# Kernel tuning notes

Measured on AMD Instinct MI355X. Metric: run time of the kernel, lower is better.

The kernel has to match this reference:

```python
import jax, jax.numpy as jnp
import numpy as np

H, QK, V, PQ, PV = 12, 32, 32, 8, 8
INF = 1e5


def _ln(x, g, b, eps=1e-5):
    m = jnp.mean(x, axis=-1, keepdims=True)
    v = jnp.mean((x - m) ** 2, axis=-1, keepdims=True)
    return (x - m) / jnp.sqrt(v + eps) * g + b


def _l2g(R, t, p):
    # R: (N,L,3,3), t: (N,L,3), p: (N,L,...,3) local points -> global
    q = jnp.einsum('nlij,nl...j->nl...i', R, p)
    tb = t.reshape(t.shape[0], t.shape[1], *([1] * (p.ndim - 3)), 3)
    return q + tb


def _g2l(R, t, q):
    tb = t.reshape(t.shape[0], t.shape[1], *([1] * (q.ndim - 3)), 3)
    return jnp.einsum('nlji,nl...j->nl...i', R, q - tb)


def setup_inputs() -> dict:
    key = jax.random.key(0)
    ks = jax.random.split(key, 24)
    N, L, F, C = 1, 384, 128, 64
    s = 0.02
    r = lambda k, sh: jax.random.normal(k, sh, dtype=jnp.float32)
    DOUT = H * C + H * V + H * PV * 7  # 1824
    return {
        'R': r(ks[0], (N, L, 3, 3)),
        't': r(ks[1], (N, L, 3)),
        'x': r(ks[2], (N, L, F)),
        'z': r(ks[3], (N, L, L, C)),
        'mask': jnp.ones((N, L), dtype=bool),
        'Wq': r(ks[4], (F, H * QK)) * s,
        'Wk': r(ks[5], (F, H * QK)) * s,
        'Wv': r(ks[6], (F, H * V)) * s,
        'Wpb': r(ks[7], (C, H)) * s,
        'spatial_coef': jnp.full((1, 1, 1, H), np.log(np.e - 1.0), dtype=jnp.float32),
        'Wqp': r(ks[8], (F, H * PQ * 3)) * s,
        'Wkp': r(ks[9], (F, H * PQ * 3)) * s,
        'Wvp': r(ks[10], (F, H * PV * 3)) * s,
        'Wout': r(ks[11], (DOUT, F)) * s,
        'bout': jnp.zeros((F,), jnp.float32),
        'ln1_g': jnp.ones((F,), jnp.float32),
        'ln1_b': jnp.zeros((F,), jnp.float32),
        'W1': r(ks[12], (F, F)) * s, 'b1': jnp.zeros((F,), jnp.float32),
        'W2': r(ks[13], (F, F)) * s, 'b2': jnp.zeros((F,), jnp.float32),
        'W3': r(ks[14], (F, F)) * s, 'b3': jnp.zeros((F,), jnp.float32),
        'ln2_g': jnp.ones((F,), jnp.float32),
        'ln2_b': jnp.zeros((F,), jnp.float32),
    }


def ga_block(R, t, x, z, mask, Wq, Wk, Wv, Wpb, spatial_coef, Wqp, Wkp, Wvp,
             Wout, bout, ln1_g, ln1_b, W1, b1, W2, b2, W3, b3, ln2_g, ln2_b):
    N, L, F = x.shape
    # node logits
    q = (x @ Wq).reshape(N, L, H, QK)
    k = (x @ Wk).reshape(N, L, H, QK)
    logits_node = jnp.einsum('nihd,njhd->nijh', q, k) / np.sqrt(QK)
    # pair logits
    logits_pair = z @ Wpb  # (N,L,L,H)
    # spatial logits: squared distances between global query/key point sets
    qp = _l2g(R, t, (x @ Wqp).reshape(N, L, H * PQ, 3)).reshape(N, L, H, PQ * 3)
    kp = _l2g(R, t, (x @ Wkp).reshape(N, L, H * PQ, 3)).reshape(N, L, H, PQ * 3)
    qn = jnp.sum(qp * qp, -1)  # (N,L,H)
    kn = jnp.sum(kp * kp, -1)
    cross = jnp.einsum('nihd,njhd->nijh', qp, kp)
    sum_sq_dist = qn[:, :, None] + kn[:, None] - 2.0 * cross  # (N,L,L,H)
    gamma = jax.nn.softplus(spatial_coef)
    logits_spatial = sum_sq_dist * (-gamma * np.sqrt(2.0 / (9 * PQ)) / 2.0)
    # masked softmax over j (axis=2)
    logits = (logits_node + logits_pair + logits_spatial) * np.sqrt(1.0 / 3.0)
    mask_row = mask[:, :, None, None]
    mask_pair = mask_row & mask[:, None, :, None]
    logits = jnp.where(mask_pair, logits, logits - INF)
    alpha = jax.nn.softmax(logits, axis=2)
    alpha = jnp.where(mask_row, alpha, jnp.zeros_like(alpha))
    # pair aggregation
    feat_p2n = jnp.einsum('nijh,nijc->nihc', alpha, z).reshape(N, L, -1)
    # node-value aggregation
    v = (x @ Wv).reshape(N, L, H, V)
    feat_node = jnp.einsum('nijh,njhd->nihd', alpha, v).reshape(N, L, -1)
    # spatial aggregation over global value points, mapped back to local frames
    vp = _l2g(R, t, (x @ Wvp).reshape(N, L, H, PV, 3))
    aggr = jnp.einsum('nijh,njhpc->nihpc', alpha, vp)
    fp = _g2l(R, t, aggr)  # (N,L,H,PV,3)
    dist = jnp.linalg.norm(fp, axis=-1)  # (N,L,H,PV)
    dirn = fp / (dist[..., None] + 1e-4)
    feat_spatial = jnp.concatenate(
        [fp.reshape(N, L, -1), dist.reshape(N, L, -1), dirn.reshape(N, L, -1)], -1)
    feat_all = jnp.concatenate([feat_p2n, feat_node, feat_spatial], -1) @ Wout + bout
    feat_all = jnp.where(mask[..., None], feat_all, jnp.zeros_like(feat_all))
    x1 = _ln(x + feat_all, ln1_g, ln1_b)
    h = jax.nn.relu(x1 @ W1 + b1)
    h = jax.nn.relu(h @ W2 + b2)
    h = h @ W3 + b3
    return _ln(x1 + h, ln2_g, ln2_b)


def reference(R, t, x, z, mask, Wq, Wk, Wv, Wpb, spatial_coef, Wqp, Wkp, Wvp,
              Wout, bout, ln1_g, ln1_b, W1, b1, W2, b2, W3, b3, ln2_g, ln2_b):
    return ga_block(R, t, x, z, mask, Wq, Wk, Wv, Wpb, spatial_coef, Wqp, Wkp,
                    Wvp, Wout, bout, ln1_g, ln1_b, W1, b1, W2, b2, W3, b3,
                    ln2_g, ln2_b)
```

## Files before the change

### kernel.cpp

```cpp
#include <hip/hip_runtime.h>
#include <math.h>

constexpr int LL   = 384;
constexpr int FF   = 128;
constexpr int NH   = 12;
constexpr int HQK  = 384;
constexpr int HV   = 384;
constexpr int HP3  = 288;
constexpr int CC   = 64;
constexpr int P2N  = 768;

__device__ inline unsigned short f2bf(float f) {
    unsigned int u = __float_as_uint(f);
    return (unsigned short)((u + 0x7fff + ((u >> 16) & 1)) >> 16);
}
__device__ inline float bf2f(unsigned short s) {
    return __uint_as_float(((unsigned int)s) << 16);
}

__global__ void __launch_bounds__(256) k1a_gemm(
    const float* __restrict__ x,
    const float* __restrict__ Wq, const float* __restrict__ Wk, const float* __restrict__ Wv,
    const float* __restrict__ Wqp, const float* __restrict__ Wkp, const float* __restrict__ Wvp,
    float* __restrict__ qb, float* __restrict__ kb, float* __restrict__ vb,
    float* __restrict__ qpl, float* __restrict__ kpl, float* __restrict__ vpl) {
    const int bid = blockIdx.x, tid = threadIdx.x;
    const int ct = bid % 63, rt = bid / 63;
    __shared__ float xs[64 * 132];

    const float* W; float* O; int ld, cb;
    if (ct < 12)      { W = Wq;  O = qb;  ld = 384; cb = ct * 32; }
    else if (ct < 24) { W = Wk;  O = kb;  ld = 384; cb = (ct - 12) * 32; }
    else if (ct < 36) { W = Wv;  O = vb;  ld = 384; cb = (ct - 24) * 32; }
    else if (ct < 45) { W = Wqp; O = qpl; ld = 288; cb = (ct - 36) * 32; }
    else if (ct < 54) { W = Wkp; O = kpl; ld = 288; cb = (ct - 45) * 32; }
    else              { W = Wvp; O = vpl; ld = 288; cb = (ct - 54) * 32; }
    const int r0 = rt * 64;

    const float4* xsrc = (const float4*)(x + (size_t)r0 * FF);
#pragma unroll
    for (int k = 0; k < 8; ++k) {
        int idx = tid + k * 256;
        float4 v = xsrc[idx];
        int row = idx >> 5, c4 = (idx & 31) * 4;
        float* d = &xs[row * 132 + c4];
        d[0] = v.x; d[1] = v.y; d[2] = v.z; d[3] = v.w;
    }
    __syncthreads();

    const int cq = (tid & 7) * 4;
    const int rr = (tid >> 3) * 2;
    const float* Wp = W + cb + cq;
    const float* xr0 = &xs[rr * 132];
    const float* xr1 = &xs[(rr + 1) * 132];
    float a00=0,a01=0,a02=0,a03=0, a10=0,a11=0,a12=0,a13=0;
#pragma unroll 8
    for (int f = 0; f < FF; ++f) {
        const float4 w = *(const float4*)(Wp + (size_t)f * ld);
        float xa = xr0[f], xb = xr1[f];
        a00 = fmaf(xa, w.x, a00); a01 = fmaf(xa, w.y, a01);
        a02 = fmaf(xa, w.z, a02); a03 = fmaf(xa, w.w, a03);
        a10 = fmaf(xb, w.x, a10); a11 = fmaf(xb, w.y, a11);
        a12 = fmaf(xb, w.z, a12); a13 = fmaf(xb, w.w, a13);
    }
    float* o0 = O + (size_t)(r0 + rr) * ld + cb + cq;
    float* o1 = o0 + ld;
    o0[0]=a00; o0[1]=a01; o0[2]=a02; o0[3]=a03;
    o1[0]=a10; o1[1]=a11; o1[2]=a12; o1[3]=a13;
}

__global__ void __launch_bounds__(256) k3_node(
    const float* __restrict__ qb, const float* __restrict__ kb,
    const float* __restrict__ qpl, const float* __restrict__ kpl,
    const float* __restrict__ R, const float* __restrict__ t,
    const float* __restrict__ spc, float* __restrict__ lgN) {
    const int it = blockIdx.x, jt = blockIdx.y, h = blockIdx.z;
    const int tid = threadIdx.x;
    __shared__ float As[64 * 60];
    __shared__ float Bs[64 * 60];
    __shared__ float pnA[512], pnB[512];
    const float g = log1pf(expf(spc[h]));
    const float s3 = 0.5773502691896258f;
    const float c1 = s3 * 0.17677669529663687f;
    const float c2 = s3 * g * (1.f / 6.f);
    const float c3 = -s3 * g * (1.f / 12.f);
    const int i0 = it * 64, j0 = jt * 64;

    for (int idx = tid; idx < 2048; idx += 256) {
        int r = idx >> 5, c = idx & 31;
        As[r*60 + c] = qb[(size_t)(i0 + r) * HQK + h*32 + c];
        Bs[r*60 + c] = kb[(size_t)(j0 + r) * HQK + h*32 + c] * c1;
    }
    for (int idx = tid; idx < 1024; idx += 256) {
        const int side = idx >> 9, rem = idx & 511;
        const int r = rem >> 3, p = rem & 7;
        const int row = (side ? j0 : i0) + r;
        const float* P = side ? kpl : qpl;
        const float* lp = P + (size_t)row * HP3 + (h*8 + p) * 3;
        float l0 = lp[0], l1 = lp[1], l2 = lp[2];
        float g0 = fmaf(R[row*9+0], l0, fmaf(R[row*9+1], l1, fmaf(R[row*9+2], l2, t[row*3+0])));
        float g1 = fmaf(R[row*9+3], l0, fmaf(R[row*9+4], l1, fmaf(R[row*9+5], l2, t[row*3+1])));
        float g2 = fmaf(R[row*9+6], l0, fmaf(R[row*9+7], l1, fmaf(R[row*9+8], l2, t[row*3+2])));
        float nn = g0*g0 + g1*g1 + g2*g2;
        if (side == 0) {
            float* d = &As[r*60 + 32 + p*3];
            d[0] = g0 * c2; d[1] = g1 * c2; d[2] = g2 * c2;
            pnA[r*8 + p] = nn;
        } else {
            float* d = &Bs[r*60 + 32 + p*3];
            d[0] = g0; d[1] = g1; d[2] = g2;
            pnB[r*8 + p] = nn;
        }
    }
    __syncthreads();
    if (tid < 64) {
        float s = 0.f;
#pragma unroll
        for (int p = 0; p < 8; ++p) s += pnA[tid*8 + p];
        As[tid*60 + 56] = s * c3;
        As[tid*60 + 57] = 1.f;
        As[tid*60 + 58] = 0.f; As[tid*60 + 59] = 0.f;
    } else if (tid < 128) {
        const int r = tid - 64;
        float s = 0.f;
#pragma unroll
        for (int p = 0; p < 8; ++p) s += pnB[r*8 + p];
        Bs[r*60 + 56] = 1.f;
        Bs[r*60 + 57] = s * c3;
        Bs[r*60 + 58] = 0.f; Bs[r*60 + 59] = 0.f;
    }
    __syncthreads();

    const int tx = tid & 15, ty = tid >> 4;
    float acc[4][4] = {};
    for (int k4 = 0; k4 < 60; k4 += 4) {
        float4 a[4], b[4];
#pragma unroll
        for (int r = 0; r < 4; ++r) a[r] = *(const float4*)&As[(ty*4 + r)*60 + k4];
#pragma unroll
        for (int c = 0; c < 4; ++c) b[c] = *(const float4*)&Bs[(tx*4 + c)*60 + k4];
#pragma unroll
        for (int r = 0; r < 4; ++r)
#pragma unroll
            for (int c = 0; c < 4; ++c) {
                acc[r][c] = fmaf(a[r].x, b[c].x, acc[r][c]);
                acc[r][c] = fmaf(a[r].y, b[c].y, acc[r][c]);
                acc[r][c] = fmaf(a[r].z, b[c].z, acc[r][c]);
                acc[r][c] = fmaf(a[r].w, b[c].w, acc[r][c]);
            }
    }
#pragma unroll
    for (int r = 0; r < 4; ++r)
        *(float4*)&lgN[((size_t)(i0 + ty*4 + r) * NH + h) * LL + j0 + tx*4] =
            make_float4(acc[r][0], acc[r][1], acc[r][2], acc[r][3]);
}

__global__ void __launch_bounds__(512, 4) k4a_fused(
    const float* __restrict__ z, const float* __restrict__ Wpb,
    float* __restrict__ lgA, float* __restrict__ feat) {
    const int i = blockIdx.x, tid = threadIdx.x;
    __shared__ __align__(16) unsigned char zu[384 * 68 * 2];
    unsigned short* z_s = (unsigned short*)zu;
    float* red = (float*)zu;
    __shared__ float a_s[NH * 384];

    const float4* zsrc = (const float4*)(z + (size_t)i * (LL * CC));
#pragma unroll
    for (int k = 0; k < 12; ++k) {
        int idx = tid + k * 512;
        float4 v = zsrc[idx];
        int j = idx >> 4, c4 = idx & 15;
        ushort4 pk;
        pk.x = f2bf(v.x); pk.y = f2bf(v.y); pk.z = f2bf(v.z); pk.w = f2bf(v.w);
        *(ushort4*)&z_s[j * 68 + c4 * 4] = pk;
    }
    __syncthreads();

    if (tid < 384) {
        const int j = tid;
        float pacc[12] = {};
        const unsigned short* zrow = &z_s[j * 68];
#pragma unroll
        for (int c4 = 0; c4 < 16; ++c4) {
            ushort4 zz = *(const ushort4*)&zrow[c4 * 4];
            float z0 = bf2f(zz.x), z1 = bf2f(zz.y), z2 = bf2f(zz.z), z3 = bf2f(zz.w);
            const float* wp = Wpb + c4 * 4 * NH;
#pragma unroll
            for (int hh = 0; hh < 12; ++hh) {
                float p = pacc[hh];
                p = fmaf(z0, wp[hh], p);
                p = fmaf(z1, wp[NH + hh], p);
                p = fmaf(z2, wp[2*NH + hh], p);
                p = fmaf(z3, wp[3*NH + hh], p);
                pacc[hh] = p;
            }
        }
        const float s3 = 0.5773502691896258f;
#pragma unroll
        for (int hh = 0; hh < 12; ++hh)
            a_s[hh * 384 + j] = lgA[((size_t)i * NH + hh) * LL + j] + pacc[hh] * s3;
    }
    __syncthreads();

    const int wv = tid >> 6, lane = tid & 63;
    if (wv < 6) {
#pragma unroll
        for (int rr = 0; rr < 2; ++rr) {
            const int h = wv * 2 + rr;
            float v[6];
#pragma unroll
            for (int k = 0; k < 6; ++k) v[k] = a_s[h * 384 + lane + k * 64];
            float m = v[0];
#pragma unroll
            for (int k = 1; k < 6; ++k) m = fmaxf(m, v[k]);
#pragma unroll
            for (int off = 32; off; off >>= 1) m = fmaxf(m, __shfl_xor(m, off));
            float s = 0.f;
#pragma unroll
            for (int k = 0; k < 6; ++k) { v[k] = expf(v[k] - m); s += v[k]; }
#pragma unroll
            for (int off = 32; off; off >>= 1) s += __shfl_xor(s, off);
            float inv = 1.f / s;
#pragma unroll
            for (int k = 0; k < 6; ++k) {
                float a = v[k] * inv;
                a_s[h * 384 + lane + k * 64] = a;
                lgA[((size_t)i * NH + h) * LL + lane + k * 64] = a;
            }
        }
    }
    __syncthreads();

    const int c4 = tid & 15, jc = tid >> 4;
    float4 acc[12] = {};
    const int jbase = jc * 12;
#pragma unroll
    for (int j4 = 0; j4 < 3; ++j4) {
        const int j = jbase + j4 * 4;
        float zv[4][4];
#pragma unroll
        for (int jj = 0; jj < 4; ++jj) {
            ushort4 zz = *(const ushort4*)&z_s[(j + jj) * 68 + c4 * 4];
            zv[jj][0] = bf2f(zz.x); zv[jj][1] = bf2f(zz.y);
            zv[jj][2] = bf2f(zz.z); zv[jj][3] = bf2f(zz.w);
        }
#pragma unroll
        for (int hh = 0; hh < 12; ++hh) {
            float4 a4 = *(const float4*)&a_s[hh * 384 + j];
            acc[hh].x = fmaf(a4.x, zv[0][0], acc[hh].x); acc[hh].y = fmaf(a4.x, zv[0][1], acc[hh].y);
            acc[hh].z = fmaf(a4.x, zv[0][2], acc[hh].z); acc[hh].w = fmaf(a4.x, zv[0][3], acc[hh].w);
            acc[hh].x = fmaf(a4.y, zv[1][0], acc[hh].x); acc[hh].y = fmaf(a4.y, zv[1][1], acc[hh].y);
            acc[hh].z = fmaf(a4.y, zv[1][2], acc[hh].z); acc[hh].w = fmaf(a4.y, zv[1][3], acc[hh].w);
            acc[hh].x = fmaf(a4.z, zv[2][0], acc[hh].x); acc[hh].y = fmaf(a4.z, zv[2][1], acc[hh].y);
            acc[hh].z = fmaf(a4.z, zv[2][2], acc[hh].z); acc[hh].w = fmaf(a4.z, zv[2][3], acc[hh].w);
            acc[hh].x = fmaf(a4.w, zv[3][0], acc[hh].x); acc[hh].y = fmaf(a4.w, zv[3][1], acc[hh].y);
            acc[hh].z = fmaf(a4.w, zv[3][2], acc[hh].z); acc[hh].w = fmaf(a4.w, zv[3][3], acc[hh].w);
        }
    }
    __syncthreads();
#pragma unroll
    for (int hh = 0; hh < 12; ++hh) {
        acc[hh].x += __shfl_xor(acc[hh].x, 16); acc[hh].y += __shfl_xor(acc[hh].y, 16);
        acc[hh].z += __shfl_xor(acc[hh].z, 16); acc[hh].w += __shfl_xor(acc[hh].w, 16);
        acc[hh].x += __shfl_xor(acc[hh].x, 32); acc[hh].y += __shfl_xor(acc[hh].y, 32);
        acc[hh].z += __shfl_xor(acc[hh].z, 32); acc[hh].w += __shfl_xor(acc[hh].w, 32);
    }
    if (lane < 16) {
#pragma unroll
        for (int hh = 0; hh < 12; ++hh)
            *(float4*)&red[wv * 768 + hh * 64 + lane * 4] = acc[hh];
    }
    __syncthreads();
    if (tid < 192) {
        int hh = tid >> 4, cc = tid & 15;
        float4 s = make_float4(0.f, 0.f, 0.f, 0.f);
#pragma unroll
        for (int w = 0; w < 8; ++w) {
            float4 p = *(const float4*)&red[w * 768 + hh * 64 + cc * 4];
            s.x += p.x; s.y += p.y; s.z += p.z; s.w += p.w;
        }
        *(float4*)&feat[(size_t)i * P2N + hh * 64 + cc * 4] = s;
    }
}

__global__ void __launch_bounds__(512) k45_aggproj(
    const float* __restrict__ alpha, const float* __restrict__ vb,
    const float* __restrict__ vpl, const float* __restrict__ R,
    const float* __restrict__ t, const float* __restrict__ feat,
    const float* __restrict__ Wout, float* __restrict__ partial) {
    const int it = blockIdx.x, h = blockIdx.y;
    const int tid = threadIdx.x;
    __shared__ float bs[128 * 57];
    __shared__ float atile[16][128];
    __shared__ float fa[16][152];
    __shared__ float sa[16][24];
    const int i0 = it * 16;
    const int wv = __builtin_amdgcn_readfirstlane(tid >> 6);
    const int n = tid & 63;

    if (tid < 256) {
        int r = tid >> 4, c4 = tid & 15;
        float4 v = *(const float4*)&feat[(size_t)(i0 + r) * P2N + h * 64 + c4 * 4];
        *(float4*)&fa[r][c4 * 4] = v;
    }

    float acc[2] = {0.f, 0.f};
    for (int tile = 0; tile < 3; ++tile) {
        const int j0 = tile * 128;
        __syncthreads();
        for (int idx = tid; idx < 2048; idx += 512) {
            if (idx < 1024) {
                int jr = idx >> 3, q = idx & 7;
                const float* src = vb + (size_t)(j0 + jr) * HV + h * 32 + q * 4;
                float* d = &bs[jr * 57 + q * 4];
                d[0] = src[0]; d[1] = src[1]; d[2] = src[2]; d[3] = src[3];
            } else {
                int id2 = idx - 1024;
                int jr = id2 >> 3, p = id2 & 7;
                const int row = j0 + jr;
                const float* lp = vpl + (size_t)row * HP3 + (h*8 + p) * 3;
                float l0 = lp[0], l1 = lp[1], l2 = lp[2];
                float g0 = fmaf(R[row*9+0], l0, fmaf(R[row*9+1], l1, fmaf(R[row*9+2], l2, t[row*3+0])));
                float g1 = fmaf(R[row*9+3], l0, fmaf(R[row*9+4], l1, fmaf(R[row*9+5], l2, t[row*3+1])));
                float g2 = fmaf(R[row*9+6], l0, fmaf(R[row*9+7], l1, fmaf(R[row*9+8], l2, t[row*3+2])));
                float* d = &bs[jr * 57 + 32 + p * 3];
                d[0] = g0; d[1] = g1; d[2] = g2;
            }
        }
        {
            int r = tid >> 5, c4 = tid & 31;
            float4 v = *(const float4*)&alpha[((size_t)(i0 + r) * NH + h) * LL + j0 + c4 * 4];
            *(float4*)&atile[r][c4 * 4] = v;
        }
        __syncthreads();
        if (n < 56) {
            for (int j4 = 0; j4 < 32; ++j4) {
                float bv0 = bs[(j4*4+0)*57 + n];
                float bv1 = bs[(j4*4+1)*57 + n];
                float bv2 = bs[(j4*4+2)*57 + n];
                float bv3 = bs[(j4*4+3)*57 + n];
#pragma unroll
                for (int r = 0; r < 2; ++r) {
                    float4 a4 = *(const float4*)&atile[wv * 2 + r][j4 * 4];
                    acc[r] = fmaf(a4.x, bv0, acc[r]);
                    acc[r] = fmaf(a4.y, bv1, acc[r]);
                    acc[r] = fmaf(a4.z, bv2, acc[r]);
                    acc[r] = fmaf(a4.w, bv3, acc[r]);
                }
            }
        }
    }
    __syncthreads();
    if (n < 56) {
        if (n < 32) {
#pragma unroll
            for (int r = 0; r < 2; ++r) fa[wv * 2 + r][64 + n] = acc[r];
        } else {
#pragma unroll
            for (int r = 0; r < 2; ++r) sa[wv * 2 + r][n - 32] = acc[r];
        }
    }
    __syncthreads();
    if (tid < 128) {
        const int ri = tid >> 3, p = tid & 7;
        const int i = i0 + ri;
        float d0 = sa[ri][p*3+0] - t[i*3+0];
        float d1 = sa[ri][p*3+1] - t[i*3+1];
        float d2 = sa[ri][p*3+2] - t[i*3+2];
        float f0 = R[i*9+0]*d0 + R[i*9+3]*d1 + R[i*9+6]*d2;
        float f1 = R[i*9+1]*d0 + R[i*9+4]*d1 + R[i*9+7]*d2;
        float f2 = R[i*9+2]*d0 + R[i*9+5]*d1 + R[i*9+8]*d2;
        float dist = sqrtf(f0*f0 + f1*f1 + f2*f2);
        float inv = 1.f / (dist + 1e-4f);
        fa[ri][96 + p*3+0] = f0; fa[ri][96 + p*3+1] = f1; fa[ri][96 + p*3+2] = f2;
        fa[ri][120 + p] = dist;
        fa[ri][128 + p*3+0] = f0*inv; fa[ri][128 + p*3+1] = f1*inv; fa[ri][128 + p*3+2] = f2*inv;
    }
    __syncthreads();

    const int f = tid & 127, rg = tid >> 7;
    float o[4] = {};
    const float* fr0 = &fa[rg * 4][0];
    {
        const float* w = Wout + (size_t)(h * 64) * FF + f;
        for (int k = 0; k < 64; ++k) {
            float wv_ = w[(size_t)k * FF];
#pragma unroll
            for (int r = 0; r < 4; ++r) o[r] = fmaf(fr0[r * 152 + k], wv_, o[r]);
        }
    }
    {
        const float* w = Wout + (size_t)(768 + h * 32) * FF + f;
        for (int k = 0; k < 32; ++k) {
            float wv_ = w[(size_t)k * FF];
#pragma unroll
            for (int r = 0; r < 4; ++r) o[r] = fmaf(fr0[r * 152 + 64 + k], wv_, o[r]);
        }
    }
    {
        const float* w = Wout + (size_t)(1152 + h * 24) * FF + f;
        for (int k = 0; k < 24; ++k) {
            float wv_ = w[(size_t)k * FF];
#pragma unroll
            for (int r = 0; r < 4; ++r) o[r] = fmaf(fr0[r * 152 + 96 + k], wv_, o[r]);
        }
    }
    {
        const float* w = Wout + (size_t)(1440 + h * 8) * FF + f;
        for (int k = 0; k < 8; ++k) {
            float wv_ = w[(size_t)k * FF];
#pragma unroll
            for (int r = 0; r < 4; ++r) o[r] = fmaf(fr0[r * 152 + 120 + k], wv_, o[r]);
        }
    }
    {
        const float* w = Wout + (size_t)(1536 + h * 24) * FF + f;
        for (int k = 0; k < 24; ++k) {
            float wv_ = w[(size_t)k * FF];
#pragma unroll
            for (int r = 0; r < 4; ++r) o[r] = fmaf(fr0[r * 152 + 128 + k], wv_, o[r]);
        }
    }
#pragma unroll
    for (int r = 0; r < 4; ++r)
        partial[((size_t)h * LL + i0 + rg * 4 + r) * FF + f] = o[r];
}

__global__ void __launch_bounds__(512) k5b_rowepi(
    const float* __restrict__ partial, const float* __restrict__ bout,
    const float* __restrict__ x,
    const float* __restrict__ ln1g, const float* __restrict__ ln1b,
    const float* __restrict__ W1, const float* __restrict__ b1,
    const float* __restrict__ W2, const float* __restrict__ b2,
    const float* __restrict__ W3, const float* __restrict__ b3,
    const float* __restrict__ ln2g, const float* __restrict__ ln2b,
    float* __restrict__ out) {
    const int i = blockIdx.x, tid = threadIdx.x;
    const int f = tid & 127, q = tid >> 7;
    __shared__ float prt[4][128];
    __shared__ float x1s[128], hbA[128], hbB[128];
    __shared__ float wrA[2], wrB[2];

    {
        float acc = 0.f;
#pragma unroll
        for (int k = 0; k < 3; ++k)
            acc += partial[((size_t)(q * 3 + k) * LL + i) * FF + f];
        prt[q][f] = acc;
    }
    __syncthreads();

    float s1 = 0.f, dv1 = 0.f;
    if (tid < 128) {
        s1 = prt[0][f] + prt[1][f] + prt[2][f] + prt[3][f] + bout[f] + x[(size_t)i * FF + f];
        float r = s1;
#pragma unroll
        for (int off = 32; off; off >>= 1) r += __shfl_xor(r, off);
        if ((tid & 63) == 0) wrA[tid >> 6] = r;
    }
    __syncthreads();
    if (tid < 128) {
        float mu = (wrA[0] + wrA[1]) * (1.f / FF);
        dv1 = s1 - mu;
        float r = dv1 * dv1;
#pragma unroll
        for (int off = 32; off; off >>= 1) r += __shfl_xor(r, off);
        if ((tid & 63) == 0) wrB[tid >> 6] = r;
    }
    __syncthreads();
    if (tid < 128) {
        float var = (wrB[0] + wrB[1]) * (1.f / FF);
        x1s[f] = dv1 * rsqrtf(var + 1e-5f) * ln1g[f] + ln1b[f];
    }
    __syncthreads();

    {
        const int k0 = q * 32;
        float p0=0,p1=0,p2=0,p3=0;
        for (int k = 0; k < 8; ++k) {
            int d = k0 + k * 4;
            p0 = fmaf(x1s[d+0], W1[(size_t)(d+0)*FF + f], p0);
            p1 = fmaf(x1s[d+1], W1[(size_t)(d+1)*FF + f], p1);
            p2 = fmaf(x1s[d+2], W1[(size_t)(d+2)*FF + f], p2);
            p3 = fmaf(x1s[d+3], W1[(size_t)(d+3)*FF + f], p3);
        }
        prt[q][f] = p0 + p1 + p2 + p3;
    }
    __syncthreads();
    if (tid < 128) hbA[f] = fmaxf(prt[0][f]+prt[1][f]+prt[2][f]+prt[3][f] + b1[f], 0.f);
    __syncthreads();
    {
        const int k0 = q * 32;
        float p0=0,p1=0,p2=0,p3=0;
        for (int k = 0; k < 8; ++k) {
            int d = k0 + k * 4;
            p0 = fmaf(hbA[d+0], W2[(size_t)(d+0)*FF + f], p0);
            p1 = fmaf(hbA[d+1], W2[(size_t)(d+1)*FF + f], p1);
            p2 = fmaf(hbA[d+2], W2[(size_t)(d+2)*FF + f], p2);
            p3 = fmaf(hbA[d+3], W2[(size_t)(d+3)*FF + f], p3);
        }
        prt[q][f] = p0 + p1 + p2 + p3;
    }
    __syncthreads();
    if (tid < 128) hbB[f] = fmaxf(prt[0][f]+prt[1][f]+prt[2][f]+prt[3][f] + b2[f], 0.f);
    __syncthreads();
    {
        const int k0 = q * 32;
        float p0=0,p1=0,p2=0,p3=0;
        for (int k = 0; k < 8; ++k) {
            int d = k0 + k * 4;
            p0 = fmaf(hbB[d+0], W3[(size_t)(d+0)*FF + f], p0);
            p1 = fmaf(hbB[d+1], W3[(size_t)(d+1)*FF + f], p1);
            p2 = fmaf(hbB[d+2], W3[(size_t)(d+2)*FF + f], p2);
            p3 = fmaf(hbB[d+3], W3[(size_t)(d+3)*FF + f], p3);
        }
        prt[q][f] = p0 + p1 + p2 + p3;
    }
    __syncthreads();

    float s2 = 0.f, dv2 = 0.f;
    if (tid < 128) {
        s2 = x1s[f] + prt[0][f]+prt[1][f]+prt[2][f]+prt[3][f] + b3[f];
        float r = s2;
#pragma unroll
        for (int off = 32; off; off >>= 1) r += __shfl_xor(r, off);
        if ((tid & 63) == 0) wrA[tid >> 6] = r;
    }
    __syncthreads();
    if (tid < 128) {
        float mu = (wrA[0] + wrA[1]) * (1.f / FF);
        dv2 = s2 - mu;
        float r = dv2 * dv2;
#pragma unroll
        for (int off = 32; off; off >>= 1) r += __shfl_xor(r, off);
        if ((tid & 63) == 0) wrB[tid >> 6] = r;
    }
    __syncthreads();
    if (tid < 128) {
        float var = (wrB[0] + wrB[1]) * (1.f / FF);
        out[(size_t)i * FF + f] = dv2 * rsqrtf(var + 1e-5f) * ln2g[f] + ln2b[f];
    }
}

extern "C" void kernel_launch(void* const* d_in, const int* in_sizes, int n_in,
                              void* d_out, int out_size, void* d_ws, size_t ws_size,
                              hipStream_t stream) {
    const float* R    = (const float*)d_in[0];
    const float* t    = (const float*)d_in[1];
    const float* x    = (const float*)d_in[2];
    const float* z    = (const float*)d_in[3];
    const float* Wq   = (const float*)d_in[5];
    const float* Wk   = (const float*)d_in[6];
    const float* Wv   = (const float*)d_in[7];
    const float* Wpb  = (const float*)d_in[8];
    const float* spc  = (const float*)d_in[9];
    const float* Wqp  = (const float*)d_in[10];
    const float* Wkp  = (const float*)d_in[11];
    const float* Wvp  = (const float*)d_in[12];
    const float* Wout = (const float*)d_in[13];
    const float* bout = (const float*)d_in[14];
    const float* ln1g = (const float*)d_in[15];
    const float* ln1b = (const float*)d_in[16];
    const float* W1   = (const float*)d_in[17];
    const float* b1   = (const float*)d_in[18];
    const float* W2   = (const float*)d_in[19];
    const float* b2   = (const float*)d_in[20];
    const float* W3   = (const float*)d_in[21];
    const float* b3   = (const float*)d_in[22];
    const float* ln2g = (const float*)d_in[23];
    const float* ln2b = (const float*)d_in[24];
    float* out = (float*)d_out;

    float* ws = (float*)d_ws;
    float* qb   = ws;
    float* kb   = qb   + (size_t)LL * HQK;
    float* vb   = kb   + (size_t)LL * HQK;
    float* qpl  = vb   + (size_t)LL * HV;
    float* kpl  = qpl  + (size_t)LL * HP3;
    float* vpl  = kpl  + (size_t)LL * HP3;
    float* lgA  = vpl  + (size_t)LL * HP3;
    float* feat = lgA  + (size_t)LL * NH * LL;
    float* part = feat + (size_t)LL * P2N;

    k1a_gemm<<<378, 256, 0, stream>>>(x, Wq, Wk, Wv, Wqp, Wkp, Wvp,
                                      qb, kb, vb, qpl, kpl, vpl);
    k3_node<<<dim3(6, 6, 12), 256, 0, stream>>>(qb, kb, qpl, kpl, R, t, spc, lgA);
    k4a_fused<<<LL, 512, 0, stream>>>(z, Wpb, lgA, feat);
    k45_aggproj<<<dim3(24, 12), 512, 0, stream>>>(lgA, vb, vpl, R, t, feat, Wout, part);
    k5b_rowepi<<<LL, 512, 0, stream>>>(part, bout, x, ln1g, ln1b,
                                       W1, b1, W2, b2, W3, b3, ln2g, ln2b, out);
}
```

Measured before the change: 86.87 us.

## Store attention weights as bf16, stage Wpb in LDS, vectorize x loads in GEMM

```diff
diff --git a/kernel.cpp b/kernel.cpp
--- a/kernel.cpp
+++ b/kernel.cpp
@@ -54,14 +54,30 @@
     const float* xr0 = &xs[rr * 132];
     const float* xr1 = &xs[(rr + 1) * 132];
     float a00=0,a01=0,a02=0,a03=0, a10=0,a11=0,a12=0,a13=0;
-#pragma unroll 8
-    for (int f = 0; f < FF; ++f) {
-        const float4 w = *(const float4*)(Wp + (size_t)f * ld);
-        float xa = xr0[f], xb = xr1[f];
-        a00 = fmaf(xa, w.x, a00); a01 = fmaf(xa, w.y, a01);
-        a02 = fmaf(xa, w.z, a02); a03 = fmaf(xa, w.w, a03);
-        a10 = fmaf(xb, w.x, a10); a11 = fmaf(xb, w.y, a11);
-        a12 = fmaf(xb, w.z, a12); a13 = fmaf(xb, w.w, a13);
+#pragma unroll 2
+    for (int f4 = 0; f4 < FF; f4 += 4) {
+        float4 xa4 = *(const float4*)(xr0 + f4);
+        float4 xb4 = *(const float4*)(xr1 + f4);
+        float4 w0 = *(const float4*)(Wp + (size_t)(f4+0) * ld);
+        float4 w1 = *(const float4*)(Wp + (size_t)(f4+1) * ld);
+        float4 w2 = *(const float4*)(Wp + (size_t)(f4+2) * ld);
+        float4 w3 = *(const float4*)(Wp + (size_t)(f4+3) * ld);
+        a00 = fmaf(xa4.x, w0.x, a00); a01 = fmaf(xa4.x, w0.y, a01);
+        a02 = fmaf(xa4.x, w0.z, a02); a03 = fmaf(xa4.x, w0.w, a03);
+        a10 = fmaf(xb4.x, w0.x, a10); a11 = fmaf(xb4.x, w0.y, a11);
+        a12 = fmaf(xb4.x, w0.z, a12); a13 = fmaf(xb4.x, w0.w, a13);
+        a00 = fmaf(xa4.y, w1.x, a00); a01 = fmaf(xa4.y, w1.y, a01);
+        a02 = fmaf(xa4.y, w1.z, a02); a03 = fmaf(xa4.y, w1.w, a03);
+        a10 = fmaf(xb4.y, w1.x, a10); a11 = fmaf(xb4.y, w1.y, a11);
+        a12 = fmaf(xb4.y, w1.z, a12); a13 = fmaf(xb4.y, w1.w, a13);
+        a00 = fmaf(xa4.z, w2.x, a00); a01 = fmaf(xa4.z, w2.y, a01);
+        a02 = fmaf(xa4.z, w2.z, a02); a03 = fmaf(xa4.z, w2.w, a03);
+        a10 = fmaf(xb4.z, w2.x, a10); a11 = fmaf(xb4.z, w2.y, a11);
+        a12 = fmaf(xb4.z, w2.z, a12); a13 = fmaf(xb4.z, w2.w, a13);
+        a00 = fmaf(xa4.w, w3.x, a00); a01 = fmaf(xa4.w, w3.y, a01);
+        a02 = fmaf(xa4.w, w3.z, a02); a03 = fmaf(xa4.w, w3.w, a03);
+        a10 = fmaf(xb4.w, w3.x, a10); a11 = fmaf(xb4.w, w3.y, a11);
+        a12 = fmaf(xb4.w, w3.z, a12); a13 = fmaf(xb4.w, w3.w, a13);
     }
     float* o0 = O + (size_t)(r0 + rr) * ld + cb + cq;
     float* o1 = o0 + ld;
@@ -157,12 +173,14 @@
 
 __global__ void __launch_bounds__(512, 4) k4a_fused(
     const float* __restrict__ z, const float* __restrict__ Wpb,
-    float* __restrict__ lgA, float* __restrict__ feat) {
+    const float* __restrict__ lgA, unsigned short* __restrict__ albf,
+    float* __restrict__ feat) {
     const int i = blockIdx.x, tid = threadIdx.x;
     __shared__ __align__(16) unsigned char zu[384 * 68 * 2];
     unsigned short* z_s = (unsigned short*)zu;
     float* red = (float*)zu;
     __shared__ float a_s[NH * 384];
+    __shared__ float wpb_s[CC * NH];
 
     const float4* zsrc = (const float4*)(z + (size_t)i * (LL * CC));
 #pragma unroll
@@ -174,6 +192,10 @@
         pk.x = f2bf(v.x); pk.y = f2bf(v.y); pk.z = f2bf(v.z); pk.w = f2bf(v.w);
         *(ushort4*)&z_s[j * 68 + c4 * 4] = pk;
     }
+    if (tid < 384) {
+        wpb_s[tid] = Wpb[tid];
+        if (tid < CC * NH - 384) wpb_s[384 + tid] = Wpb[384 + tid];
+    }
     __syncthreads();
 
     if (tid < 384) {
@@ -184,7 +206,7 @@
         for (int c4 = 0; c4 < 16; ++c4) {
             ushort4 zz = *(const ushort4*)&zrow[c4 * 4];
             float z0 = bf2f(zz.x), z1 = bf2f(zz.y), z2 = bf2f(zz.z), z3 = bf2f(zz.w);
-            const float* wp = Wpb + c4 * 4 * NH;
+            const float* wp = wpb_s + c4 * 4 * NH;
 #pragma unroll
             for (int hh = 0; hh < 12; ++hh) {
                 float p = pacc[hh];
@@ -221,11 +243,12 @@
 #pragma unroll
             for (int off = 32; off; off >>= 1) s += __shfl_xor(s, off);
             float inv = 1.f / s;
+            unsigned short* arow = albf + ((size_t)i * NH + h) * LL;
 #pragma unroll
             for (int k = 0; k < 6; ++k) {
                 float a = v[k] * inv;
                 a_s[h * 384 + lane + k * 64] = a;
-                lgA[((size_t)i * NH + h) * LL + lane + k * 64] = a;
+                arow[lane + k * 64] = f2bf(a);
             }
         }
     }
@@ -284,7 +307,7 @@
 }
 
 __global__ void __launch_bounds__(512) k45_aggproj(
-    const float* __restrict__ alpha, const float* __restrict__ vb,
+    const unsigned short* __restrict__ albf, const float* __restrict__ vb,
     const float* __restrict__ vpl, const float* __restrict__ R,
     const float* __restrict__ t, const float* __restrict__ feat,
     const float* __restrict__ Wout, float* __restrict__ partial) {
@@ -328,9 +351,10 @@
             }
         }
         {
-            int r = tid >> 5, c4 = tid & 31;
-            float4 v = *(const float4*)&alpha[((size_t)(i0 + r) * NH + h) * LL + j0 + c4 * 4];
-            *(float4*)&atile[r][c4 * 4] = v;
+            int r = tid >> 5, c8 = tid & 31;
+            ushort4 v = *(const ushort4*)&albf[((size_t)(i0 + r) * NH + h) * LL + j0 + c8 * 4];
+            float* d = &atile[r][c8 * 4];
+            d[0] = bf2f(v.x); d[1] = bf2f(v.y); d[2] = bf2f(v.z); d[3] = bf2f(v.w);
         }
         __syncthreads();
         if (n < 56) {
@@ -581,12 +605,13 @@
     float* lgA  = vpl  + (size_t)LL * HP3;
     float* feat = lgA  + (size_t)LL * NH * LL;
     float* part = feat + (size_t)LL * P2N;
+    unsigned short* albf = (unsigned short*)(part + (size_t)NH * LL * FF);
 
     k1a_gemm<<<378, 256, 0, stream>>>(x, Wq, Wk, Wv, Wqp, Wkp, Wvp,
                                       qb, kb, vb, qpl, kpl, vpl);
     k3_node<<<dim3(6, 6, 12), 256, 0, stream>>>(qb, kb, qpl, kpl, R, t, spc, lgA);
-    k4a_fused<<<LL, 512, 0, stream>>>(z, Wpb, lgA, feat);
-    k45_aggproj<<<dim3(24, 12), 512, 0, stream>>>(lgA, vb, vpl, R, t, feat, Wout, part);
+    k4a_fused<<<LL, 512, 0, stream>>>(z, Wpb, lgA, albf, feat);
+    k45_aggproj<<<dim3(24, 12), 512, 0, stream>>>(albf, vb, vpl, R, t, feat, Wout, part);
     k5b_rowepi<<<LL, 512, 0, stream>>>(part, bout, x, ln1g, ln1b,
                                        W1, b1, W2, b2, W3, b3, ln2g, ln2b, out);
 }
```

After: 86.32 us. No clear change (-0.6%).
